# Optimization experiments

Measured on AMD Instinct MI355X. Metric: run time of the kernel, lower is better.

Reference implementation:

```python
import jax, jax.numpy as jnp
import numpy as np

N, E, R = 50000, 320000, 3
IN, HID, OUT = 768, 256, 64
NEG_SLOPE = 0.2


def _rgat_conv(x, src, dst, edge_type, W, q, k, bias):
    # x: [N, HID]; W: [R, HID, HID]; q,k: [HID, 1]; bias: [HID]
    n = x.shape[0]
    xw = jnp.einsum('nc,rco->rno', x, W)          # [R, N, HID] per-relation transform
    out_i = xw[edge_type, dst]                      # [E, HID] transformed target feats
    out_j = xw[edge_type, src]                      # [E, HID] transformed source feats
    alpha = jax.nn.leaky_relu(out_i @ q + out_j @ k, NEG_SLOPE)  # [E, 1]
    # across-relation segment softmax over destination nodes (PyG softmax semantics)
    m = jax.ops.segment_max(alpha, dst, num_segments=n)          # [N, 1]
    ea = jnp.exp(alpha - m[dst])
    denom = jax.ops.segment_sum(ea, dst, num_segments=n)         # [N, 1]
    a = ea / (denom[dst] + 1e-16)                                # [E, 1]
    out = jax.ops.segment_sum(a * out_j, dst, num_segments=n)    # [N, HID]
    return out + bias


def setup_inputs() -> dict:
    key = jax.random.key(0)
    ks = jax.random.split(key, 16)
    g = lambda k, shape, fan: (jax.random.normal(k, shape, jnp.float32) / np.float32(np.sqrt(fan)))
    return {
        'x': jax.random.normal(ks[0], (N, IN), jnp.float32),
        'edge_index': jax.random.randint(ks[1], (2, E), 0, N),
        'edge_type': jax.random.randint(ks[2], (E,), 0, R),
        'w_in': g(ks[3], (IN, HID), IN), 'b_in': jnp.zeros((HID,), jnp.float32),
        'conv1_w': g(ks[4], (R, HID, HID), HID),
        'conv1_q': g(ks[5], (HID, 1), HID),
        'conv1_k': g(ks[6], (HID, 1), HID),
        'conv1_b': jnp.zeros((HID,), jnp.float32),
        'conv2_w': g(ks[7], (R, HID, HID), HID),
        'conv2_q': g(ks[8], (HID, 1), HID),
        'conv2_k': g(ks[9], (HID, 1), HID),
        'conv2_b': jnp.zeros((HID,), jnp.float32),
        'w_out': g(ks[10], (HID, OUT), HID), 'b_out': jnp.zeros((OUT,), jnp.float32),
        'w_cls': g(ks[11], (OUT, 2), OUT), 'b_cls': jnp.zeros((2,), jnp.float32),
    }


def reference(x, edge_index, edge_type, w_in, b_in,
              conv1_w, conv1_q, conv1_k, conv1_b,
              conv2_w, conv2_q, conv2_k, conv2_b,
              w_out, b_out, w_cls, b_cls):
    src, dst = edge_index[0], edge_index[1]
    h = jax.nn.relu(x @ w_in + b_in)                                  # [N, HID]
    h = _rgat_conv(h, src, dst, edge_type, conv1_w, conv1_q, conv1_k, conv1_b)
    h = _rgat_conv(h, src, dst, edge_type, conv2_w, conv2_q, conv2_k, conv2_b)
    h = jax.nn.relu(h @ w_out + b_out)                                # [N, OUT]
    return h @ w_cls + b_cls                                          # [N, 2]
```

## Files before the change

kernel.cpp:

```cpp
#include <hip/hip_runtime.h>
#include <hip/hip_bf16.h>

#define RG86_NN 50000
#define RG86_NE 320000
#define RG86_NR 3
#define RG86_DIN 768
#define RG86_HID 256
#define RG86_OUT 64

typedef __bf16 rg_bv8 __attribute__((ext_vector_type(8)));
typedef short rg_sv8 __attribute__((ext_vector_type(8)));
typedef float rg_fv4 __attribute__((ext_vector_type(4)));

static __device__ float rg_b2f(unsigned short u) {
  return __uint_as_float(((unsigned int)u) << 16);
}
static __device__ unsigned short rg_f2b(float f) {
  unsigned int u = __float_as_uint(f);
  u += 0x7FFFu + ((u >> 16) & 1u);
  return (unsigned short)(u >> 16);
}

__global__ void RGATModel_86371792322702_kernel() {}

__global__ void rg_cast(const float* in, unsigned short* out, int n) {
  int i = (blockIdx.x * 256 + threadIdx.x) * 4;
  if (i < n) {
    float4 v = *(const float4*)(in + i);
    ushort4 o = make_ushort4(rg_f2b(v.x), rg_f2b(v.y), rg_f2b(v.z), rg_f2b(v.w));
    *(ushort4*)(out + i) = o;
  }
}

__global__ void rg_castT(const float* in, unsigned short* out, int rows, int cols) {
  int i = blockIdx.x * 256 + threadIdx.x;
  if (i < rows * cols) {
    int r = i / cols, c = i % cols;
    out[(size_t)c * rows + r] = rg_f2b(in[i]);
  }
}

__global__ void rg_gemm_m(const unsigned short* A, const unsigned short* Bt,
                          const float* bias, unsigned short* C,
                          int M, int N, int K, int relu, int mblk) {
  __shared__ unsigned short sA[64][40];
  __shared__ unsigned short sB[64][40];
  int tid = threadIdx.x;
  int wave = tid >> 6, lane = tid & 63;
  int m0 = (blockIdx.x % mblk) * 64, n0 = (blockIdx.x / mblk) * 64;
  int lr = tid >> 2, lk = (tid & 3) * 8;
  int frow = lane & 15, fk = (lane >> 4) * 8;
  rg_fv4 acc[4] = {};
  for (int k0 = 0; k0 < K; k0 += 32) {
    rg_sv8 av = {};
    if (m0 + lr < M) av = *(const rg_sv8*)(A + (size_t)(m0 + lr) * K + k0 + lk);
    *(rg_sv8*)&sA[lr][lk] = av;
    rg_sv8 bv = *(const rg_sv8*)(Bt + (size_t)(n0 + lr) * K + k0 + lk);
    *(rg_sv8*)&sB[lr][lk] = bv;
    __syncthreads();
    rg_bv8 a = *(const rg_bv8*)&sA[wave * 16 + frow][fk];
#pragma unroll
    for (int t = 0; t < 4; t++) {
      rg_bv8 b = *(const rg_bv8*)&sB[t * 16 + frow][fk];
      acc[t] = __builtin_amdgcn_mfma_f32_16x16x32_bf16(a, b, acc[t], 0, 0, 0);
    }
    __syncthreads();
  }
  int orow = m0 + wave * 16 + (lane >> 4) * 4;
  int ocol = n0 + (lane & 15);
  for (int t = 0; t < 4; t++) {
    int col = ocol + t * 16;
    float bv = bias ? bias[col] : 0.f;
    for (int r = 0; r < 4; r++) {
      int row = orow + r;
      if (row < M) {
        float v = acc[t][r] + bv;
        if (relu && v < 0.f) v = 0.f;
        C[(size_t)row * N + col] = rg_f2b(v);
      }
    }
  }
}

__global__ void rg_hist(const int* d, int* counts) {
  int e = blockIdx.x * 256 + threadIdx.x;
  if (e < RG86_NE) atomicAdd(&counts[d[e]], 1);
}

__global__ void rg_scan1(const int* counts, int* tmp, int* bsum, int n) {
  int b = blockIdx.x, t = threadIdx.x;
  int base = b * 1024 + t * 4;
  int v0 = 0, v1 = 0, v2 = 0, v3 = 0;
  if (base + 3 < n) {
    int4 v = *(const int4*)(counts + base);
    v0 = v.x; v1 = v.y; v2 = v.z; v3 = v.w;
  } else {
    if (base + 0 < n) v0 = counts[base + 0];
    if (base + 1 < n) v1 = counts[base + 1];
    if (base + 2 < n) v2 = counts[base + 2];
    if (base + 3 < n) v3 = counts[base + 3];
  }
  int tsum = v0 + v1 + v2 + v3;
  int lane = t & 63, wave = t >> 6;
  int s = tsum;
  for (int off = 1; off < 64; off <<= 1) {
    int u = __shfl_up(s, off);
    if (lane >= off) s += u;
  }
  __shared__ int wsum[4];
  if (lane == 63) wsum[wave] = s;
  __syncthreads();
  int woff = 0;
  for (int w = 0; w < wave; w++) woff += wsum[w];
  int excl = woff + s - tsum;
  int e0 = excl, e1 = e0 + v0, e2 = e1 + v1, e3 = e2 + v2;
  if (base + 3 < n) {
    *(int4*)(tmp + base) = make_int4(e0, e1, e2, e3);
  } else {
    if (base + 0 < n) tmp[base + 0] = e0;
    if (base + 1 < n) tmp[base + 1] = e1;
    if (base + 2 < n) tmp[base + 2] = e2;
    if (base + 3 < n) tmp[base + 3] = e3;
  }
  if (t == 255) bsum[b] = woff + s;
}

__global__ void rg_scan2(int* bsum, int* rowptr, int nb, int n) {
  int lane = threadIdx.x;
  int v = (lane < nb) ? bsum[lane] : 0;
  int s = v;
  for (int off = 1; off < 64; off <<= 1) {
    int u = __shfl_up(s, off);
    if (lane >= off) s += u;
  }
  if (lane < nb) bsum[lane] = s - v;
  if (lane == 63) rowptr[n] = s;
}

__global__ void rg_scan3(const int* bsum, int* rowptr, int* cursor, int n) {
  int b = blockIdx.x, t = threadIdx.x;
  int base = b * 1024 + t * 4;
  int off = bsum[b];
  if (base + 3 < n) {
    int4 v = *(const int4*)(cursor + base);
    int4 o = make_int4(v.x + off, v.y + off, v.z + off, v.w + off);
    *(int4*)(rowptr + base) = o;
    *(int4*)(cursor + base) = o;
  } else {
    for (int j = 0; j < 4; j++)
      if (base + j < n) {
        int o = cursor[base + j] + off;
        rowptr[base + j] = o;
        cursor[base + j] = o;
      }
  }
}

__global__ void rg_scatter(const int* d, int* cursor, int* perm) {
  int e = blockIdx.x * 256 + threadIdx.x;
  if (e < RG86_NE) perm[atomicAdd(&cursor[d[e]], 1)] = e;
}

__global__ void rg_qk(const unsigned short* xw, const float* q, const float* k,
                      float* qd, float* kd) {
  int lane = threadIdx.x & 63;
  int p = blockIdx.x * 4 + (threadIdx.x >> 6);
  if (p >= RG86_NR * RG86_NN) return;
  const unsigned short* xr = xw + (size_t)p * RG86_HID + lane * 4;
  float qv = 0.f, kv = 0.f;
  for (int j = 0; j < 4; j++) {
    float xv = rg_b2f(xr[j]);
    qv += xv * q[lane * 4 + j];
    kv += xv * k[lane * 4 + j];
  }
  for (int o = 32; o >= 1; o >>= 1) { qv += __shfl_xor(qv, o); kv += __shfl_xor(kv, o); }
  if (lane == 0) { qd[p] = qv; kd[p] = kv; }
}

__global__ void rg_edge(const int* perm, const int* src, const int* dst,
                        const int* et, const float* qd, const float* kd,
                        float* alphap, int* srcrel) {
  int i = blockIdx.x * 256 + threadIdx.x;
  if (i >= RG86_NE) return;
  int e = perm[i];
  int t = et[e], sv = src[e], dv = dst[e];
  float al = qd[t * RG86_NN + dv] + kd[t * RG86_NN + sv];
  al = al > 0.f ? al : 0.2f * al;
  alphap[i] = al;
  srcrel[i] = t * RG86_NN + sv;
}

__global__ void rg_agg(const int* rowptr, const float* alphap, const int* srcrel,
                       const unsigned short* xw, const float* bias,
                       unsigned short* out) {
  __shared__ float sw[4][64];
  __shared__ int ssrc[4][64];
  int lane = threadIdx.x & 63;
  int wv = threadIdx.x >> 6;
  int node = blockIdx.x * 4 + wv;
  if (node >= RG86_NN) return;
  int s0 = rowptr[node], s1 = rowptr[node + 1];
  int c0 = lane * 4;
  float a0 = 0.f, a1 = 0.f, a2 = 0.f, a3 = 0.f;
  if (s1 > s0) {
    float m = -1e30f;
    for (int bs = s0; bs < s1; bs += 64) {
      int i = bs + lane;
      float al = (i < s1) ? alphap[i] : -1e30f;
      m = fmaxf(m, al);
    }
    for (int o = 32; o >= 1; o >>= 1) m = fmaxf(m, __shfl_xor(m, o));
    float den = 0.f;
    for (int bs = s0; bs < s1; bs += 64) {
      int i = bs + lane;
      if (i < s1) den += __expf(alphap[i] - m);
    }
    for (int o = 32; o >= 1; o >>= 1) den += __shfl_xor(den, o);
    float inv = 1.f / (den + 1e-16f);
    for (int bs = s0; bs < s1; bs += 64) {
      int i = bs + lane;
      int nch = s1 - bs; if (nch > 64) nch = 64;
      float w = 0.f; int sr = 0;
      if (i < s1) { w = __expf(alphap[i] - m) * inv; sr = srcrel[i]; }
      sw[wv][lane] = w;
      ssrc[wv][lane] = sr;
#pragma unroll 4
      for (int j = 0; j < nch; j++) {
        float wj = sw[wv][j];
        ushort4 v = *(const ushort4*)(xw + (size_t)ssrc[wv][j] * RG86_HID + c0);
        a0 += wj * rg_b2f(v.x);
        a1 += wj * rg_b2f(v.y);
        a2 += wj * rg_b2f(v.z);
        a3 += wj * rg_b2f(v.w);
      }
    }
  }
  unsigned short* op = out + (size_t)node * RG86_HID + c0;
  op[0] = rg_f2b(a0 + bias[c0 + 0]);
  op[1] = rg_f2b(a1 + bias[c0 + 1]);
  op[2] = rg_f2b(a2 + bias[c0 + 2]);
  op[3] = rg_f2b(a3 + bias[c0 + 3]);
}

__global__ void rg_cls(const unsigned short* h4, const float* wc, const float* bc,
                       float* out) {
  int n = blockIdx.x * 256 + threadIdx.x;
  if (n >= RG86_NN) return;
  float a0 = bc[0], a1 = bc[1];
  const unsigned short* hr = h4 + (size_t)n * RG86_OUT;
  for (int j = 0; j < RG86_OUT; j++) {
    float h = rg_b2f(hr[j]);
    a0 += h * wc[j * 2 + 0];
    a1 += h * wc[j * 2 + 1];
  }
  out[n * 2 + 0] = a0;
  out[n * 2 + 1] = a1;
}

extern "C" void kernel_launch(void* const* d_in, const int* in_sizes, int n_in,
                              void* d_out, int out_size, void* d_ws, size_t ws_size,
                              hipStream_t stream) {
  (void)in_sizes; (void)n_in; (void)out_size;
  const float* x = (const float*)d_in[0];
  const int* ei = (const int*)d_in[1];
  const int* etp = (const int*)d_in[2];
  const float* w_in = (const float*)d_in[3];
  const float* b_in = (const float*)d_in[4];
  const float* c1w = (const float*)d_in[5];
  const float* c1q = (const float*)d_in[6];
  const float* c1k = (const float*)d_in[7];
  const float* c1b = (const float*)d_in[8];
  const float* c2w = (const float*)d_in[9];
  const float* c2q = (const float*)d_in[10];
  const float* c2k = (const float*)d_in[11];
  const float* c2b = (const float*)d_in[12];
  const float* w_out = (const float*)d_in[13];
  const float* b_out = (const float*)d_in[14];
  const float* w_cls = (const float*)d_in[15];
  const float* b_cls = (const float*)d_in[16];
  const int* esrc = ei;
  const int* edst = ei + RG86_NE;

  char* base = (char*)d_ws;
  size_t off = 0;
  unsigned short* xb = (unsigned short*)(base + off);
  unsigned short* xw = xb;
  off += (size_t)RG86_NN * RG86_DIN * 2;
  unsigned short* h1b = (unsigned short*)(base + off); off += (size_t)RG86_NN * RG86_HID * 2;
  unsigned short* h2b = (unsigned short*)(base + off); off += (size_t)RG86_NN * RG86_HID * 2;
  unsigned short* h4b = (unsigned short*)(base + off); off += (size_t)RG86_NN * RG86_OUT * 2;
  unsigned short* w_inT = (unsigned short*)(base + off); off += (size_t)RG86_DIN * RG86_HID * 2;
  unsigned short* c1wT = (unsigned short*)(base + off); off += (size_t)RG86_NR * RG86_HID * RG86_HID * 2;
  unsigned short* c2wT = (unsigned short*)(base + off); off += (size_t)RG86_NR * RG86_HID * RG86_HID * 2;
  unsigned short* w_outT = (unsigned short*)(base + off); off += (size_t)RG86_HID * RG86_OUT * 2;
  float* qd = (float*)(base + off); off += (size_t)RG86_NR * RG86_NN * 4;
  float* kd = (float*)(base + off); off += (size_t)RG86_NR * RG86_NN * 4;
  int* counts = (int*)(base + off); off += (size_t)RG86_NN * 4;
  int* rowptr = (int*)(base + off); off += (size_t)(RG86_NN + 4) * 4;
  int* cursor = (int*)(base + off); off += (size_t)RG86_NN * 4;
  int* perm = (int*)(base + off); off += (size_t)RG86_NE * 4;
  int* bsum = (int*)(base + off); off += (size_t)64 * 4;
  float* alphap = (float*)(base + off); off += (size_t)RG86_NE * 4;
  int* srcrel = (int*)(base + off); off += (size_t)RG86_NE * 4;
  if (off > ws_size) return;

  int mblk = (RG86_NN + 63) / 64;
  int gh = mblk * (RG86_HID / 64);
  int nsb = (RG86_NN + 1023) / 1024;

  rg_cast<<<(RG86_NN * RG86_DIN / 4 + 255) / 256, 256, 0, stream>>>(
      x, xb, RG86_NN * RG86_DIN);
  rg_castT<<<(RG86_DIN * RG86_HID + 255) / 256, 256, 0, stream>>>(
      w_in, w_inT, RG86_DIN, RG86_HID);
  for (int r = 0; r < RG86_NR; r++) {
    rg_castT<<<(RG86_HID * RG86_HID + 255) / 256, 256, 0, stream>>>(
        c1w + (size_t)r * RG86_HID * RG86_HID,
        c1wT + (size_t)r * RG86_HID * RG86_HID, RG86_HID, RG86_HID);
    rg_castT<<<(RG86_HID * RG86_HID + 255) / 256, 256, 0, stream>>>(
        c2w + (size_t)r * RG86_HID * RG86_HID,
        c2wT + (size_t)r * RG86_HID * RG86_HID, RG86_HID, RG86_HID);
  }
  rg_castT<<<(RG86_HID * RG86_OUT + 255) / 256, 256, 0, stream>>>(
      w_out, w_outT, RG86_HID, RG86_OUT);

  rg_gemm_m<<<gh, 256, 0, stream>>>(xb, w_inT, b_in, h1b,
                                    RG86_NN, RG86_HID, RG86_DIN, 1, mblk);

  hipMemsetAsync(counts, 0, (size_t)RG86_NN * 4, stream);
  rg_hist<<<(RG86_NE + 255) / 256, 256, 0, stream>>>(edst, counts);
  rg_scan1<<<nsb, 256, 0, stream>>>(counts, cursor, bsum, RG86_NN);
  rg_scan2<<<1, 64, 0, stream>>>(bsum, rowptr, nsb, RG86_NN);
  rg_scan3<<<nsb, 256, 0, stream>>>(bsum, rowptr, cursor, RG86_NN);
  rg_scatter<<<(RG86_NE + 255) / 256, 256, 0, stream>>>(edst, cursor, perm);

  for (int r = 0; r < RG86_NR; r++)
    rg_gemm_m<<<gh, 256, 0, stream>>>(h1b, c1wT + (size_t)r * RG86_HID * RG86_HID,
                                      (const float*)0,
                                      xw + (size_t)r * RG86_NN * RG86_HID,
                                      RG86_NN, RG86_HID, RG86_HID, 0, mblk);
  rg_qk<<<(RG86_NR * RG86_NN + 3) / 4, 256, 0, stream>>>(xw, c1q, c1k, qd, kd);
  rg_edge<<<(RG86_NE + 255) / 256, 256, 0, stream>>>(perm, esrc, edst, etp, qd, kd,
                                                     alphap, srcrel);
  rg_agg<<<(RG86_NN + 3) / 4, 256, 0, stream>>>(rowptr, alphap, srcrel,
                                                xw, c1b, h2b);

  for (int r = 0; r < RG86_NR; r++)
    rg_gemm_m<<<gh, 256, 0, stream>>>(h2b, c2wT + (size_t)r * RG86_HID * RG86_HID,
                                      (const float*)0,
                                      xw + (size_t)r * RG86_NN * RG86_HID,
                                      RG86_NN, RG86_HID, RG86_HID, 0, mblk);
  rg_qk<<<(RG86_NR * RG86_NN + 3) / 4, 256, 0, stream>>>(xw, c2q, c2k, qd, kd);
  rg_edge<<<(RG86_NE + 255) / 256, 256, 0, stream>>>(perm, esrc, edst, etp, qd, kd,
                                                     alphap, srcrel);
  rg_agg<<<(RG86_NN + 3) / 4, 256, 0, stream>>>(rowptr, alphap, srcrel,
                                                xw, c2b, h1b);

  rg_gemm_m<<<mblk, 256, 0, stream>>>(h1b, w_outT, b_out, h4b,
                                      RG86_NN, RG86_OUT, RG86_HID, 1, mblk);

  rg_cls<<<(RG86_NN + 255) / 256, 256, 0, stream>>>(h4b, w_cls, b_cls, (float*)d_out);
}
```

Before: 689.5 us.

## Rewrite GEMM with 128x64 tiles, direct-to-LDS loads, swizzle and fused relations

Replaces the 64x64, K=32 bf16 GEMM with a 128x64, K=64 tile kernel. The new kernel loads global memory straight into LDS with global_load_lds, uses an XOR-swizzled LDS layout to avoid bank conflicts, and remaps workgroups across the XCDs. The three per-relation GEMMs become one launch over N=768 that writes a relation-split output layout, and the per-relation weight transposes are merged into one kernel per layer. The aim is more data reuse per tile, fewer launches and less LDS staging overhead. The cost is more register pressure, and the clamped row reads on the last M tile load redundant data.

Measured after the change: 586.1 us. 15.0% less time.

```diff
diff --git a/kernel.cpp b/kernel.cpp
--- a/kernel.cpp
+++ b/kernel.cpp
@@ -11,6 +11,7 @@
 typedef __bf16 rg_bv8 __attribute__((ext_vector_type(8)));
 typedef short rg_sv8 __attribute__((ext_vector_type(8)));
 typedef float rg_fv4 __attribute__((ext_vector_type(4)));
+typedef unsigned int rg_u32;
 
 static __device__ float rg_b2f(unsigned short u) {
   return __uint_as_float(((unsigned int)u) << 16);
@@ -19,6 +20,13 @@
   unsigned int u = __float_as_uint(f);
   u += 0x7FFFu + ((u >> 16) & 1u);
   return (unsigned short)(u >> 16);
+}
+
+static __device__ __forceinline__ void rg_gl16(const void* g, void* lds_wave_base) {
+  __builtin_amdgcn_global_load_lds(
+      (const __attribute__((address_space(1))) rg_u32*)(unsigned long long)(uintptr_t)g,
+      (__attribute__((address_space(3))) rg_u32*)(unsigned int)(uintptr_t)lds_wave_base,
+      16, 0, 0);
 }
 
 __global__ void RGATModel_86371792322702_kernel() {}
@@ -40,43 +48,90 @@
   }
 }
 
-__global__ void rg_gemm_m(const unsigned short* A, const unsigned short* Bt,
-                          const float* bias, unsigned short* C,
-                          int M, int N, int K, int relu, int mblk) {
-  __shared__ unsigned short sA[64][40];
-  __shared__ unsigned short sB[64][40];
+__global__ void rg_castT3(const float* in, unsigned short* out) {
+  int i = blockIdx.x * 256 + threadIdx.x;
+  if (i < RG86_NR * RG86_HID * RG86_HID) {
+    int r = i >> 16, j = i & 65535;
+    int row = j >> 8, col = j & 255;
+    out[(r << 16) + (col << 8) + row] = rg_f2b(in[i]);
+  }
+}
+
+__global__ __launch_bounds__(256) void rg_gemm2(
+    const unsigned short* A, const unsigned short* Bt, const float* bias,
+    unsigned short* C, int M, int N, int K, int relu, int split) {
+  __shared__ unsigned short sA[128 * 64];
+  __shared__ unsigned short sB[64 * 64];
   int tid = threadIdx.x;
-  int wave = tid >> 6, lane = tid & 63;
-  int m0 = (blockIdx.x % mblk) * 64, n0 = (blockIdx.x / mblk) * 64;
-  int lr = tid >> 2, lk = (tid & 3) * 8;
-  int frow = lane & 15, fk = (lane >> 4) * 8;
-  rg_fv4 acc[4] = {};
-  for (int k0 = 0; k0 < K; k0 += 32) {
-    rg_sv8 av = {};
-    if (m0 + lr < M) av = *(const rg_sv8*)(A + (size_t)(m0 + lr) * K + k0 + lk);
-    *(rg_sv8*)&sA[lr][lk] = av;
-    rg_sv8 bv = *(const rg_sv8*)(Bt + (size_t)(n0 + lr) * K + k0 + lk);
-    *(rg_sv8*)&sB[lr][lk] = bv;
+  int wv = tid >> 6, lane = tid & 63;
+  int nwg = gridDim.x;
+  int q = nwg >> 3, rres = nwg & 7;
+  int xcd = blockIdx.x & 7, jj = blockIdx.x >> 3;
+  int wg = (xcd < rres ? xcd * (q + 1) : rres * (q + 1) + (xcd - rres) * q) + jj;
+  int ntiles = N >> 6;
+  int mt = wg / ntiles, nt = wg - mt * ntiles;
+  int m0 = mt * 128, n0 = nt * 64;
+  int frow = lane & 15, fhi = lane >> 4;
+  rg_fv4 acc[2][4] = {};
+  for (int k0 = 0; k0 < K; k0 += 64) {
+#pragma unroll
+    for (int i = 0; i < 4; i++) {
+      int idx = i * 256 + tid;
+      int r = idx >> 3, s = idx & 7;
+      int gr = m0 + r;
+      if (gr >= M) gr = M - 1;
+      const unsigned short* gp = A + (size_t)gr * K + k0 + ((s ^ (r & 7)) << 3);
+      rg_gl16(gp, (char*)sA + (size_t)(i * 256 + wv * 64) * 16);
+    }
+#pragma unroll
+    for (int i = 0; i < 2; i++) {
+      int idx = i * 256 + tid;
+      int r = idx >> 3, s = idx & 7;
+      const unsigned short* gp = Bt + (size_t)(n0 + r) * K + k0 + ((s ^ (r & 7)) << 3);
+      rg_gl16(gp, (char*)sB + (size_t)(i * 256 + wv * 64) * 16);
+    }
     __syncthreads();
-    rg_bv8 a = *(const rg_bv8*)&sA[wave * 16 + frow][fk];
-#pragma unroll
-    for (int t = 0; t < 4; t++) {
-      rg_bv8 b = *(const rg_bv8*)&sB[t * 16 + frow][fk];
-      acc[t] = __builtin_amdgcn_mfma_f32_16x16x32_bf16(a, b, acc[t], 0, 0, 0);
+#pragma unroll
+    for (int ks = 0; ks < 2; ks++) {
+      rg_bv8 af[2], bf[4];
+#pragma unroll
+      for (int mf = 0; mf < 2; mf++) {
+        int r = wv * 32 + mf * 16 + frow;
+        int slot = (ks * 4 + fhi) ^ (r & 7);
+        af[mf] = *(const rg_bv8*)((const char*)sA + r * 128 + slot * 16);
+      }
+#pragma unroll
+      for (int nf = 0; nf < 4; nf++) {
+        int r = nf * 16 + frow;
+        int slot = (ks * 4 + fhi) ^ (r & 7);
+        bf[nf] = *(const rg_bv8*)((const char*)sB + r * 128 + slot * 16);
+      }
+#pragma unroll
+      for (int mf = 0; mf < 2; mf++)
+#pragma unroll
+        for (int nf = 0; nf < 4; nf++)
+          acc[mf][nf] = __builtin_amdgcn_mfma_f32_16x16x32_bf16(af[mf], bf[nf],
+                                                                acc[mf][nf], 0, 0, 0);
     }
     __syncthreads();
   }
-  int orow = m0 + wave * 16 + (lane >> 4) * 4;
-  int ocol = n0 + (lane & 15);
-  for (int t = 0; t < 4; t++) {
-    int col = ocol + t * 16;
-    float bv = bias ? bias[col] : 0.f;
-    for (int r = 0; r < 4; r++) {
-      int row = orow + r;
-      if (row < M) {
-        float v = acc[t][r] + bv;
-        if (relu && v < 0.f) v = 0.f;
-        C[(size_t)row * N + col] = rg_f2b(v);
+#pragma unroll
+  for (int mf = 0; mf < 2; mf++) {
+#pragma unroll
+    for (int nf = 0; nf < 4; nf++) {
+      int col = n0 + nf * 16 + frow;
+      float bv = bias ? bias[col] : 0.f;
+#pragma unroll
+      for (int r = 0; r < 4; r++) {
+        int row = m0 + wv * 32 + mf * 16 + fhi * 4 + r;
+        if (row < M) {
+          float v = acc[mf][nf][r] + bv;
+          if (relu && v < 0.f) v = 0.f;
+          if (split)
+            C[((size_t)(col >> 8) * RG86_NN + row) * 256 + (col & 255)] = rg_f2b(v);
+          else
+            C[(size_t)row * N + col] = rg_f2b(v);
+        }
       }
     }
   }
@@ -304,27 +359,20 @@
   int* srcrel = (int*)(base + off); off += (size_t)RG86_NE * 4;
   if (off > ws_size) return;
 
-  int mblk = (RG86_NN + 63) / 64;
-  int gh = mblk * (RG86_HID / 64);
+  int mt128 = (RG86_NN + 127) / 128;
   int nsb = (RG86_NN + 1023) / 1024;
 
   rg_cast<<<(RG86_NN * RG86_DIN / 4 + 255) / 256, 256, 0, stream>>>(
       x, xb, RG86_NN * RG86_DIN);
   rg_castT<<<(RG86_DIN * RG86_HID + 255) / 256, 256, 0, stream>>>(
       w_in, w_inT, RG86_DIN, RG86_HID);
-  for (int r = 0; r < RG86_NR; r++) {
-    rg_castT<<<(RG86_HID * RG86_HID + 255) / 256, 256, 0, stream>>>(
-        c1w + (size_t)r * RG86_HID * RG86_HID,
-        c1wT + (size_t)r * RG86_HID * RG86_HID, RG86_HID, RG86_HID);
-    rg_castT<<<(RG86_HID * RG86_HID + 255) / 256, 256, 0, stream>>>(
-        c2w + (size_t)r * RG86_HID * RG86_HID,
-        c2wT + (size_t)r * RG86_HID * RG86_HID, RG86_HID, RG86_HID);
-  }
+  rg_castT3<<<(RG86_NR * RG86_HID * RG86_HID + 255) / 256, 256, 0, stream>>>(c1w, c1wT);
+  rg_castT3<<<(RG86_NR * RG86_HID * RG86_HID + 255) / 256, 256, 0, stream>>>(c2w, c2wT);
   rg_castT<<<(RG86_HID * RG86_OUT + 255) / 256, 256, 0, stream>>>(
       w_out, w_outT, RG86_HID, RG86_OUT);
 
-  rg_gemm_m<<<gh, 256, 0, stream>>>(xb, w_inT, b_in, h1b,
-                                    RG86_NN, RG86_HID, RG86_DIN, 1, mblk);
+  rg_gemm2<<<mt128 * 4, 256, 0, stream>>>(xb, w_inT, b_in, h1b,
+                                          RG86_NN, RG86_HID, RG86_DIN, 1, 0);
 
   hipMemsetAsync(counts, 0, (size_t)RG86_NN * 4, stream);
   rg_hist<<<(RG86_NE + 255) / 256, 256, 0, stream>>>(edst, counts);
@@ -333,30 +381,24 @@
   rg_scan3<<<nsb, 256, 0, stream>>>(bsum, rowptr, cursor, RG86_NN);
   rg_scatter<<<(RG86_NE + 255) / 256, 256, 0, stream>>>(edst, cursor, perm);
 
-  for (int r = 0; r < RG86_NR; r++)
-    rg_gemm_m<<<gh, 256, 0, stream>>>(h1b, c1wT + (size_t)r * RG86_HID * RG86_HID,
-                                      (const float*)0,
-                                      xw + (size_t)r * RG86_NN * RG86_HID,
-                                      RG86_NN, RG86_HID, RG86_HID, 0, mblk);
+  rg_gemm2<<<mt128 * 12, 256, 0, stream>>>(h1b, c1wT, (const float*)0, xw,
+                                           RG86_NN, RG86_NR * RG86_HID, RG86_HID, 0, 1);
   rg_qk<<<(RG86_NR * RG86_NN + 3) / 4, 256, 0, stream>>>(xw, c1q, c1k, qd, kd);
   rg_edge<<<(RG86_NE + 255) / 256, 256, 0, stream>>>(perm, esrc, edst, etp, qd, kd,
                                                      alphap, srcrel);
   rg_agg<<<(RG86_NN + 3) / 4, 256, 0, stream>>>(rowptr, alphap, srcrel,
                                                 xw, c1b, h2b);
 
-  for (int r = 0; r < RG86_NR; r++)
-    rg_gemm_m<<<gh, 256, 0, stream>>>(h2b, c2wT + (size_t)r * RG86_HID * RG86_HID,
-                                      (const float*)0,
-                                      xw + (size_t)r * RG86_NN * RG86_HID,
-                                      RG86_NN, RG86_HID, RG86_HID, 0, mblk);
+  rg_gemm2<<<mt128 * 12, 256, 0, stream>>>(h2b, c2wT, (const float*)0, xw,
+                                           RG86_NN, RG86_NR * RG86_HID, RG86_HID, 0, 1);
   rg_qk<<<(RG86_NR * RG86_NN + 3) / 4, 256, 0, stream>>>(xw, c2q, c2k, qd, kd);
   rg_edge<<<(RG86_NE + 255) / 256, 256, 0, stream>>>(perm, esrc, edst, etp, qd, kd,
                                                      alphap, srcrel);
   rg_agg<<<(RG86_NN + 3) / 4, 256, 0, stream>>>(rowptr, alphap, srcrel,
                                                 xw, c2b, h1b);
 
-  rg_gemm_m<<<mblk, 256, 0, stream>>>(h1b, w_outT, b_out, h4b,
-                                      RG86_NN, RG86_OUT, RG86_HID, 1, mblk);
+  rg_gemm2<<<mt128, 256, 0, stream>>>(h1b, w_outT, b_out, h4b,
+                                      RG86_NN, RG86_OUT, RG86_HID, 1, 0);
 
   rg_cls<<<(RG86_NN + 255) / 256, 256, 0, stream>>>(h4b, w_cls, b_cls, (float*)d_out);
 }
```
